# Kernel optimization log

Measured on AMD Instinct MI355X. Metric: run time of the kernel, lower is better.

Reference implementation:

```python
import jax, jax.numpy as jnp
import numpy as np

L, N, E, H, D = 2048, 4, 1024, 16, 128  # seq, batch, embed, heads, proj_dim
HD = E // H                             # head_dim = 64
SIGMA = 1.0
EPS = 1e-6


def setup_inputs() -> dict:
    key = jax.random.key(0)
    ks = jax.random.split(key, 13)
    w = lambda i, shape: jax.random.normal(ks[i], shape, jnp.float32) * 0.02
    return {
        "query": jax.random.normal(ks[0], (L, N, E), jnp.float32),
        "key": jax.random.normal(ks[1], (L, N, E), jnp.float32),
        "value": jax.random.normal(ks[2], (L, N, E), jnp.float32),
        "wq": w(3, (E, E)), "bq": jnp.zeros((E,), jnp.float32),
        "wk": w(4, (E, E)), "bk": jnp.zeros((E,), jnp.float32),
        "wv": w(5, (E, E)), "bv": jnp.zeros((E,), jnp.float32),
        "wo": w(6, (E, E)), "bo": jnp.zeros((E,), jnp.float32),
        "random_matrices": SIGMA * jax.random.normal(ks[7], (H, D, HD), jnp.float32),
    }


def random_project(x, rm):
    # x: (L, N, H, HD), rm: (H, D, HD) -> phi: (N*H, L, 2D)
    scale = 1.0 / np.sqrt(2 * D).astype(np.float32)
    xn = x / jnp.maximum(jnp.linalg.norm(x, axis=-1, keepdims=True), 1e-12)
    xt = jnp.einsum('lnhe,hde->lnhd', xn, rm)
    phi = scale * jnp.concatenate([jnp.exp(xt), jnp.exp(-xt)], axis=-1)  # (L,N,H,2D)
    # faithful to torch .contiguous().view(-1, L, 2D): plain row-major reshape
    return phi.reshape(N * H, L, 2 * D)


def causal_product(phi_q, phi_k, v):
    # phi_q, phi_k: (B, L, 2D); v: (B, L, HD)
    B = phi_q.shape[0]
    def step(carry, inp):
        S, z = carry            # S: (B, 2D, HD) running kv; z: (B, 2D) running k-sum
        qk, kk, vv = inp        # (B, 2D), (B, 2D), (B, HD)
        S = S + kk[:, :, None] * vv[:, None, :]
        z = z + kk
        num = jnp.einsum('bd,bdh->bh', qk, S)
        den = jnp.einsum('bd,bd->b', qk, z)
        return (S, z), num / (den[:, None] + EPS)
    init = (jnp.zeros((B, 2 * D, HD), phi_q.dtype), jnp.zeros((B, 2 * D), phi_q.dtype))
    xs = (jnp.swapaxes(phi_q, 0, 1), jnp.swapaxes(phi_k, 0, 1), jnp.swapaxes(v, 0, 1))
    _, out = jax.lax.scan(step, init, xs)   # out: (L, B, HD)
    return jnp.swapaxes(out, 0, 1)          # (B, L, HD)


def reference(query, key, value, wq, bq, wk, bk, wv, bv, wo, bo, random_matrices):
    q = query @ wq.T + bq
    k = key @ wk.T + bk
    v = value @ wv.T + bv
    q = q.reshape(L, N, H, HD)
    k = k.reshape(L, N, H, HD)
    v = jnp.swapaxes(v.reshape(L, N * H, HD), 0, 1)   # (B=N*H, L, HD)
    phi_q = random_project(q, random_matrices)        # (B, L, 2D)
    phi_k = random_project(k, random_matrices)
    attn = causal_product(phi_q, phi_k, v)            # (B, L, HD)
    attn = jnp.swapaxes(attn, 0, 1).reshape(L, N, E)
    return attn @ wo.T + bo
```

## Files before the change

kernel.cpp:

```cpp
#include <hip/hip_runtime.h>
#include <math.h>


typedef unsigned short u16;
typedef unsigned int u32;
using f32x4v  = __attribute__((ext_vector_type(4))) float;
using f32x16v = __attribute__((ext_vector_type(16))) float;
using s16x8   = __attribute__((ext_vector_type(8))) short;

__device__ __forceinline__ float bf2f(u16 u) { return __uint_as_float(((u32)u) << 16); }
__device__ __forceinline__ u16 f2bf(float x) {
    u32 b = __float_as_uint(x);
    b += 0x7fff + ((b >> 16) & 1);
    return (u16)(b >> 16);
}
__device__ __forceinline__ u32 cvtpk(float lo, float hi) {
    u32 r;
    asm("v_cvt_pk_bf16_f32 %0, %1, %2" : "=v"(r) : "v"(lo), "v"(hi));
    return r;
}
__device__ __forceinline__ float exp2f_hw(float x) {
    float r;
    asm("v_exp_f32 %0, %1" : "=v"(r) : "v"(x));
    return r;
}
__device__ __forceinline__ void gload_lds16(const void* g, void* l) {
    __builtin_amdgcn_global_load_lds(
        (const __attribute__((address_space(1))) void*)g,
        (__attribute__((address_space(3))) void*)l, 16, 0, 0);
}

__global__ __launch_bounds__(256) void cvt_consts(
    const float* __restrict__ w0, const float* __restrict__ w1,
    const float* __restrict__ w2, const float* __restrict__ w3,
    const float* __restrict__ rm, const float* __restrict__ query,
    const float* __restrict__ key, u16* __restrict__ wqkv,
    u16* __restrict__ wob, u16* __restrict__ rmb,
    u16* __restrict__ xq, u16* __restrict__ xk)
{
    const int y = blockIdx.y;
    const float* src;
    u16* d;
    int nblk;
    switch (y) {
        case 0: src = w0; d = wqkv;            nblk = 512;  break;
        case 1: src = w1; d = wqkv + 1048576;  nblk = 512;  break;
        case 2: src = w2; d = wqkv + 2097152;  nblk = 512;  break;
        case 3: src = w3; d = wob;             nblk = 512;  break;
        case 4: src = rm; d = rmb;             nblk = 64;   break;
        case 5: src = query; d = xq;           nblk = 4096; break;
        default: src = key; d = xk;            nblk = 4096; break;
    }
    if ((int)blockIdx.x >= nblk) return;
    const size_t i = ((size_t)blockIdx.x * 256 + threadIdx.x) * 8;
    const float4 a = *(const float4*)(src + i);
    const float4 b = *(const float4*)(src + i + 4);
    u16 o[8] = {f2bf(a.x), f2bf(a.y), f2bf(a.z), f2bf(a.w),
                f2bf(b.x), f2bf(b.y), f2bf(b.z), f2bf(b.w)};
    *(uint4*)(d + i) = *(uint4*)o;
}

__global__ __launch_bounds__(256) void gemm_qkv(
    const u16* __restrict__ XQ, const u16* __restrict__ XK, const float* __restrict__ Xv,
    const u16* __restrict__ WB, const float* __restrict__ bq, const float* __restrict__ bk,
    const float* __restrict__ bv, u16* __restrict__ qp, u16* __restrict__ kp, u16* __restrict__ vpt)
{
    __shared__ __align__(16) u16 As[8192];
    __shared__ __align__(16) u16 Bs[8192];
    const int z = blockIdx.z;
    const u16* Bw = WB + (size_t)z * 1048576;
    const float* bias = (z == 0) ? bq : (z == 1) ? bk : bv;

    const int t = threadIdx.x;
    const int m0 = blockIdx.x * 128, n0 = blockIdx.y * 128;
    const int wid = t >> 6, lane = t & 63;
    const int wr = wid >> 1, wc = wid & 1;
    const int l15 = lane & 15, l4 = lane >> 4;

    f32x4v acc[4][4];
#pragma unroll
    for (int i = 0; i < 4; ++i)
#pragma unroll
        for (int j = 0; j < 4; ++j)
#pragma unroll
            for (int e = 0; e < 4; ++e) acc[i][j][e] = 0.f;

    const int grow = wid * 32 + (lane >> 3);
    const int lcol = ((lane & 7) ^ (lane >> 3)) * 8;
    const u16* gbB = Bw + (size_t)(n0 + grow) * 1024 + lcol;
    const u16* XA  = (z == 0) ? XQ : XK;
    const u16* gaA = XA + (size_t)(m0 + grow) * 1024 + lcol;
    const int srow = t >> 1;
    const int half = t & 1;
    const float* gsrcA = Xv + (size_t)(m0 + srow) * 1024 + half * 32;

    for (int k0 = 0; k0 < 1024; k0 += 64) {
        __syncthreads();
#pragma unroll
        for (int i = 0; i < 4; ++i)
            gload_lds16(gbB + (size_t)i * 8 * 1024 + k0, &Bs[(wid * 32 + i * 8) * 64]);
        if (z < 2) {
#pragma unroll
            for (int i = 0; i < 4; ++i)
                gload_lds16(gaA + (size_t)i * 8 * 1024 + k0, &As[(wid * 32 + i * 8) * 64]);
        } else {
            u16 ta[32];
#pragma unroll
            for (int q = 0; q < 8; ++q) {
                const float4 v = *(const float4*)(gsrcA + k0 + q * 4);
                ta[q*4+0] = f2bf(v.x); ta[q*4+1] = f2bf(v.y);
                ta[q*4+2] = f2bf(v.z); ta[q*4+3] = f2bf(v.w);
            }
#pragma unroll
            for (int q = 0; q < 4; ++q) {
                const int phys = (half * 4 + q) ^ (srow & 7);
                *(uint4*)&As[srow * 64 + phys * 8] = *(const uint4*)&ta[q * 8];
            }
        }
        __syncthreads();
#pragma unroll
        for (int ks = 0; ks < 2; ++ks) {
            s16x8 af[4], bfr[4];
#pragma unroll
            for (int fi = 0; fi < 4; ++fi) {
                const int r = wr * 64 + fi * 16 + l15;
                const int phys = (ks * 4 + l4) ^ (r & 7);
                af[fi] = *(const s16x8*)&As[r * 64 + phys * 8];
            }
#pragma unroll
            for (int fj = 0; fj < 4; ++fj) {
                const int r = wc * 64 + fj * 16 + l15;
                const int phys = (ks * 4 + l4) ^ (r & 7);
                bfr[fj] = *(const s16x8*)&Bs[r * 64 + phys * 8];
            }
#pragma unroll
            for (int fi = 0; fi < 4; ++fi)
#pragma unroll
                for (int fj = 0; fj < 4; ++fj)
                    acc[fi][fj] = __builtin_amdgcn_mfma_f32_16x16x32_bf16(af[fi], bfr[fj], acc[fi][fj], 0, 0, 0);
        }
    }

    u16* Cp = (z == 0) ? qp : (z == 1) ? kp : vpt;
    const int rl = l4 * 4, cl = l15;
    float bvals[4];
#pragma unroll
    for (int fj = 0; fj < 4; ++fj) bvals[fj] = bias[n0 + wc * 64 + fj * 16 + cl];
#pragma unroll
    for (int fi = 0; fi < 4; ++fi)
#pragma unroll
        for (int j = 0; j < 4; ++j) {
            const size_t m = m0 + wr * 64 + fi * 16 + rl + j;
#pragma unroll
            for (int fj = 0; fj < 4; ++fj) {
                const int n = n0 + wc * 64 + fj * 16 + cl;
                const float v = acc[fi][fj][j] + bvals[fj];
                if (z < 2) Cp[m * 1024 + n] = f2bf(v);
                else       Cp[((size_t)((m & 3) * 16 + (n >> 6)) * 64 + (n & 63)) * 2048 + (m >> 2)] = f2bf(v);
            }
        }
}

__global__ __launch_bounds__(256) void gemm_o(
    const u16* __restrict__ A, const u16* __restrict__ Bw,
    const float* __restrict__ bias, float* __restrict__ Cp)
{
    __shared__ __align__(16) u16 As[8192];
    __shared__ __align__(16) u16 Bs[8192];
    const int t = threadIdx.x;
    const int m0 = blockIdx.x * 128, n0 = blockIdx.y * 128;
    const int wid = t >> 6, lane = t & 63;
    const int wr = wid >> 1, wc = wid & 1;
    const int l15 = lane & 15, l4 = lane >> 4;

    f32x4v acc[4][4];
#pragma unroll
    for (int i = 0; i < 4; ++i)
#pragma unroll
        for (int j = 0; j < 4; ++j)
#pragma unroll
            for (int e = 0; e < 4; ++e) acc[i][j][e] = 0.f;

    const int grow = wid * 32 + (lane >> 3);
    const int lcol = ((lane & 7) ^ (lane >> 3)) * 8;
    const u16* gaA = A  + (size_t)(m0 + grow) * 1024 + lcol;
    const u16* gbB = Bw + (size_t)(n0 + grow) * 1024 + lcol;

    for (int k0 = 0; k0 < 1024; k0 += 64) {
        __syncthreads();
#pragma unroll
        for (int i = 0; i < 4; ++i) {
            gload_lds16(gaA + (size_t)i * 8 * 1024 + k0, &As[(wid * 32 + i * 8) * 64]);
            gload_lds16(gbB + (size_t)i * 8 * 1024 + k0, &Bs[(wid * 32 + i * 8) * 64]);
        }
        __syncthreads();
#pragma unroll
        for (int ks = 0; ks < 2; ++ks) {
            s16x8 af[4], bfr[4];
#pragma unroll
            for (int fi = 0; fi < 4; ++fi) {
                const int r = wr * 64 + fi * 16 + l15;
                const int phys = (ks * 4 + l4) ^ (r & 7);
                af[fi] = *(const s16x8*)&As[r * 64 + phys * 8];
            }
#pragma unroll
            for (int fj = 0; fj < 4; ++fj) {
                const int r = wc * 64 + fj * 16 + l15;
                const int phys = (ks * 4 + l4) ^ (r & 7);
                bfr[fj] = *(const s16x8*)&Bs[r * 64 + phys * 8];
            }
#pragma unroll
            for (int fi = 0; fi < 4; ++fi)
#pragma unroll
                for (int fj = 0; fj < 4; ++fj)
                    acc[fi][fj] = __builtin_amdgcn_mfma_f32_16x16x32_bf16(af[fi], bfr[fj], acc[fi][fj], 0, 0, 0);
        }
    }

    const int rl = l4 * 4, cl = l15;
    float bvals[4];
#pragma unroll
    for (int fj = 0; fj < 4; ++fj) bvals[fj] = bias[n0 + wc * 64 + fj * 16 + cl];
#pragma unroll
    for (int fi = 0; fi < 4; ++fi)
#pragma unroll
        for (int j = 0; j < 4; ++j) {
            const size_t m = m0 + wr * 64 + fi * 16 + rl + j;
#pragma unroll
            for (int fj = 0; fj < 4; ++fj) {
                const int n = n0 + wc * 64 + fj * 16 + cl;
                Cp[m * 1024 + n] = acc[fi][fj][j] + bvals[fj];
            }
        }
}

__global__ __launch_bounds__(256) void rand_project_mfma(
    const u16* __restrict__ QP, const u16* __restrict__ KP,
    const u16* __restrict__ RMB, u16* __restrict__ PHIQ, u16* __restrict__ PHIK)
{
    const u16* X  = (blockIdx.z == 0) ? QP : KP;
    u16* PHI      = (blockIdx.z == 0) ? PHIQ : PHIK;
    __shared__ __align__(16) u16 Xs[128 * 72];
    __shared__ __align__(16) u16 RMs[128 * 72];
    __shared__ float rsl_lds[128];
    const int h  = blockIdx.x;
    const int r0 = blockIdx.y * 128;
    const int t  = threadIdx.x;
    const int w  = t >> 6, lane = t & 63;
    const int l15 = lane & 15, l4 = lane >> 4;

    float sq[4];
#pragma unroll
    for (int i = 0; i < 4; ++i) {
        const int lin = t + i * 256;
        const int row = lin >> 3, oct = lin & 7;
        const uint4 xv = *(const uint4*)(X + (size_t)(r0 + row) * 1024 + h * 64 + oct * 8);
        *(uint4*)&Xs[row * 72 + oct * 8] = xv;
        const u16* pv = (const u16*)&xv;
        float s = 0.f;
#pragma unroll
        for (int e = 0; e < 8; ++e) { const float f = bf2f(pv[e]); s += f * f; }
        sq[i] = s;
        const uint4 rv = *(const uint4*)(RMB + (size_t)h * 8192 + lin * 8);
        *(uint4*)&RMs[row * 72 + oct * 8] = rv;
    }
#pragma unroll
    for (int i = 0; i < 4; ++i) {
        sq[i] += __shfl_xor(sq[i], 1);
        sq[i] += __shfl_xor(sq[i], 2);
        sq[i] += __shfl_xor(sq[i], 4);
        if ((t & 7) == 0)
            rsl_lds[(t >> 3) + i * 32] = 1.4426950408889634f / fmaxf(sqrtf(sq[i]), 1e-12f);
    }
    __syncthreads();

    const int wr = (w >> 1) * 64, wc = (w & 1) * 64;
    f32x4v acc[4][4];
#pragma unroll
    for (int i = 0; i < 4; ++i)
#pragma unroll
        for (int j = 0; j < 4; ++j)
#pragma unroll
            for (int e = 0; e < 4; ++e) acc[i][j][e] = 0.f;
#pragma unroll
    for (int ks = 0; ks < 2; ++ks) {
        s16x8 af[4], bfr[4];
#pragma unroll
        for (int fi = 0; fi < 4; ++fi)
            af[fi] = *(const s16x8*)&Xs[(wr + fi * 16 + l15) * 72 + ks * 32 + l4 * 8];
#pragma unroll
        for (int fj = 0; fj < 4; ++fj)
            bfr[fj] = *(const s16x8*)&RMs[(wc + fj * 16 + l15) * 72 + ks * 32 + l4 * 8];
#pragma unroll
        for (int fi = 0; fi < 4; ++fi)
#pragma unroll
            for (int fj = 0; fj < 4; ++fj)
                acc[fi][fj] = __builtin_amdgcn_mfma_f32_16x16x32_bf16(af[fi], bfr[fj], acc[fi][fj], 0, 0, 0);
    }

#pragma unroll
    for (int fi = 0; fi < 4; ++fi)
#pragma unroll
        for (int reg = 0; reg < 4; ++reg) {
            const int row = wr + fi * 16 + l4 * 4 + reg;
            const float rsl = rsl_lds[row];
            const size_t base = ((size_t)(r0 + row) * 16 + h) * 256;
#pragma unroll
            for (int fj = 0; fj < 4; ++fj) {
                const int d = wc + fj * 16 + l15;
                const float arg = acc[fi][fj][reg] * rsl;
                PHI[base + d]       = f2bf(exp2f_hw(arg - 4.f));
                PHI[base + 128 + d] = f2bf(exp2f_hw(-arg - 4.f));
            }
        }
}

__global__ __launch_bounds__(256) void chunk_state_mfma(
    const u16* __restrict__ PHIK, const u16* __restrict__ VPT, u16* __restrict__ STC)
{
    __shared__ __align__(16) u16 Ks[64 * 136];
    __shared__ float zlds[16][132];
    const int b = blockIdx.x;
    const int c = blockIdx.y >> 1;
    const int dh = blockIdx.y & 1;
    const int t = threadIdx.x;
    const int wid = t >> 6, lane = t & 63;
    const int l15 = lane & 15, l4 = lane >> 4;
    const int wr = wid >> 1, wc = wid & 1;

    const size_t R0 = (size_t)b * 2048 + (size_t)c * 256;
    const int rgrp = t >> 4, d08 = (t & 15) * 8;

    float zpart[8];
#pragma unroll
    for (int i = 0; i < 8; ++i) zpart[i] = 0.f;

    f32x4v acc[2][4];
#pragma unroll
    for (int i = 0; i < 2; ++i)
#pragma unroll
        for (int j = 0; j < 4; ++j)
#pragma unroll
            for (int e = 0; e < 4; ++e) acc[i][j][e] = 0.f;

    for (int stage = 0; stage < 4; ++stage) {
        __syncthreads();
#pragma unroll
        for (int j = 0; j < 4; ++j) {
            const int r = rgrp + 16 * j;
            const uint4 v = *(const uint4*)(PHIK + (R0 + stage * 64 + r) * 256 + dh * 128 + d08);
            const int x = ((r >> 3) & 3) << 1;
            *(uint4*)&Ks[r * 136 + (((d08 >> 3) ^ x) << 3)] = v;
            const u16* pv = (const u16*)&v;
#pragma unroll
            for (int i = 0; i < 8; ++i) zpart[i] += bf2f(pv[i]);
        }
        __syncthreads();
#pragma unroll
        for (int ks = 0; ks < 2; ++ks) {
            const int xk = ((ks * 4 + l4) & 3) << 1;
            const int r0 = ks * 32 + l4 * 8;
            s16x8 af[2], bk[4];
#pragma unroll
            for (int fi = 0; fi < 2; ++fi) {
                const int h = wr * 32 + fi * 16 + l15;
                af[fi] = *(const s16x8*)(VPT + ((size_t)b * 64 + h) * 2048 + c * 256 + stage * 64 + ks * 32 + l4 * 8);
            }
#pragma unroll
            for (int fj = 0; fj < 4; ++fj) {
                const int d = wc * 64 + fj * 16 + l15;
                const int colk = (((d >> 3) ^ xk) << 3) + (d & 7);
#pragma unroll
                for (int e = 0; e < 8; ++e)
                    bk[fj][e] = (short)Ks[(r0 + e) * 136 + colk];
            }
#pragma unroll
            for (int fi = 0; fi < 2; ++fi)
#pragma unroll
                for (int fj = 0; fj < 4; ++fj)
                    acc[fi][fj] = __builtin_amdgcn_mfma_f32_16x16x32_bf16(af[fi], bk[fj], acc[fi][fj], 0, 0, 0);
        }
    }
    __syncthreads();
    *(float4*)&zlds[rgrp][d08]     = *(float4*)&zpart[0];
    *(float4*)&zlds[rgrp][d08 + 4] = *(float4*)&zpart[4];
    __syncthreads();
    u16* st = STC + (size_t)(b * 8 + c) * 16640;
    if (t < 128) {
        float z = 0.f;
#pragma unroll
        for (int g = 0; g < 16; ++g) z += zlds[g][t];
        st[16384 + dh * 128 + t] = f2bf(z);
    }
#pragma unroll
    for (int fi = 0; fi < 2; ++fi)
#pragma unroll
        for (int reg = 0; reg < 4; ++reg) {
            const int h = wr * 32 + fi * 16 + l4 * 4 + reg;
#pragma unroll
            for (int fj = 0; fj < 4; ++fj) {
                const int d = dh * 128 + wc * 64 + fj * 16 + l15;
                st[(size_t)h * 256 + d] = f2bf(acc[fi][fj][reg]);
            }
        }
}

__global__ void prefix_scan(const u16* __restrict__ STC, u16* __restrict__ STBF)
{
    const int b = blockIdx.x;
    const int e = blockIdx.y * 256 + threadIdx.x;
    if (e >= 16640) return;
    float run = 0.f;
#pragma unroll
    for (int c = 0; c < 8; ++c) {
        const size_t idx = (size_t)(b * 8 + c) * 16640 + e;
        const float v = bf2f(STC[idx]);
        STBF[idx] = f2bf(run);
        run += v;
    }
}

__global__ __launch_bounds__(128) void causal_fused(
    const u16* __restrict__ PHIQ, const u16* __restrict__ PHIK,
    const u16* __restrict__ VPT, const u16* __restrict__ STBF,
    u16* __restrict__ ATT)
{
    const u32 bid = blockIdx.x;
    const int pair = (int)((bid >> 3) & 3);
    const int G  = (int)((bid >> 5) * 8 + (bid & 7));
    const int b  = G & 63;
    const int c  = G >> 6;
    const int w  = threadIdx.x >> 6;
    const int rf = w ? (7 - pair) : pair;
    const int ri = rf >> 1, fi = rf & 1;
    const int lane = threadIdx.x & 63;
    const int l31 = lane & 31, s = lane >> 5;
    const size_t chunk0 = (size_t)b * 2048 + (size_t)c * 256;
    const u16* stb = STBF + (size_t)(b * 8 + c) * 16640;

    const int qc = ri * 64 + fi * 32 + l31;
    s16x8 qf[16];
    const u16* qp = PHIQ + (chunk0 + qc) * 256 + s * 8;
#pragma unroll
    for (int ds = 0; ds < 16; ++ds)
        qf[ds] = *(const s16x8*)(qp + ds * 16);

    f32x16v o[2], o2;
#pragma unroll
    for (int e = 0; e < 16; ++e) { o[0][e] = 0.f; o[1][e] = 0.f; o2[e] = 0.f; }
    float den = 0.f;

#pragma unroll
    for (int ds = 0; ds < 16; ++ds) {
        const s16x8 zf = *(const s16x8*)(stb + 16384 + ds * 16 + s * 8);
        o2 = __builtin_amdgcn_mfma_f32_32x32x16_bf16(qf[ds], zf, o2, 0, 0, 0);
#pragma unroll
        for (int fh = 0; fh < 2; ++fh) {
            const s16x8 sx = *(const s16x8*)(stb + (fh * 32 + l31) * 256 + ds * 16 + s * 8);
            o[fh] = __builtin_amdgcn_mfma_f32_32x32x16_bf16(qf[ds], sx, o[fh], 0, 0, 0);
        }
    }

    const int kbmax = ri * 2 + fi;
    for (int kb = 0; kb <= kbmax; ++kb) {
        s16x8 vf[2][2];
#pragma unroll
        for (int kh = 0; kh < 2; ++kh)
#pragma unroll
            for (int fh = 0; fh < 2; ++fh)
                vf[kh][fh] = *(const s16x8*)(VPT + ((size_t)b * 64 + fh * 32 + l31) * 2048
                                             + c * 256 + kb * 32 + kh * 16 + s * 8);
        f32x16v p0, p1;
#pragma unroll
        for (int e = 0; e < 16; ++e) { p0[e] = 0.f; p1[e] = 0.f; }
        const u16* kptr = PHIK + (chunk0 + kb * 32 + l31) * 256 + s * 8;
#pragma unroll
        for (int ds = 0; ds < 8; ++ds) {
            const s16x8 kf0 = *(const s16x8*)(kptr + (2 * ds) * 16);
            const s16x8 kf1 = *(const s16x8*)(kptr + (2 * ds + 1) * 16);
            p0 = __builtin_amdgcn_mfma_f32_32x32x16_bf16(kf0, qf[2 * ds],     p0, 0, 0, 0);
            p1 = __builtin_amdgcn_mfma_f32_32x32x16_bf16(kf1, qf[2 * ds + 1], p1, 0, 0, 0);
        }
        f32x16v p;
#pragma unroll
        for (int e = 0; e < 16; ++e) p[e] = p0[e] + p1[e];

        const bool diag = (kb == kbmax);
        float rsum = 0.f;
#pragma unroll
        for (int reg = 0; reg < 16; ++reg) {
            if (diag) {
                const int kc = kb * 32 + (reg & 3) + 8 * (reg >> 2) + 4 * s;
                if (kc > qc) p[reg] = 0.f;
            }
            rsum += p[reg];
        }
        den += rsum;
#pragma unroll
        for (int kh = 0; kh < 2; ++kh) {
            const u32 pA_lo = cvtpk(p[8*kh + 0], p[8*kh + 1]);
            const u32 pA_hi = cvtpk(p[8*kh + 2], p[8*kh + 3]);
            const u32 pB_lo = cvtpk(p[8*kh + 4], p[8*kh + 5]);
            const u32 pB_hi = cvtpk(p[8*kh + 6], p[8*kh + 7]);
            const u32 X_lo = s ? pB_lo : pA_lo;
            const u32 X_hi = s ? pB_hi : pA_hi;
            const u32 Y_lo = s ? pA_lo : pB_lo;
            const u32 Y_hi = s ? pA_hi : pB_hi;
            const u32 sY_lo = __shfl_xor((int)Y_lo, 32);
            const u32 sY_hi = __shfl_xor((int)Y_hi, 32);
            u32 wq[4];
            wq[0] = s ? sY_lo : X_lo;
            wq[1] = s ? sY_hi : X_hi;
            wq[2] = s ? X_lo : sY_lo;
            wq[3] = s ? X_hi : sY_hi;
            s16x8 pa;
#pragma unroll
            for (int i = 0; i < 4; ++i) {
                pa[2*i]   = (short)(wq[i] & 0xffff);
                pa[2*i+1] = (short)(wq[i] >> 16);
            }
            o[0] = __builtin_amdgcn_mfma_f32_32x32x16_bf16(pa, vf[kh][0], o[0], 0, 0, 0);
            o[1] = __builtin_amdgcn_mfma_f32_32x32x16_bf16(pa, vf[kh][1], o[1], 0, 0, 0);
        }
    }

    const float denT = den + __shfl_xor(den, 32);
#pragma unroll
    for (int reg = 0; reg < 16; ++reg) {
        const int q32 = (reg & 3) + 8 * (reg >> 2) + 4 * s;
        const float dv = o2[reg] + __shfl(denT, q32);
        const float inv = 1.f / (dv + 1e-6f);
        const int qrow = c * 256 + ri * 64 + fi * 32 + q32;
        const size_t abase = (size_t)qrow * 4096 + b * 64;
        ATT[abase + l31]      = f2bf(o[0][reg] * inv);
        ATT[abase + 32 + l31] = f2bf(o[1][reg] * inv);
    }
}

extern "C" void kernel_launch(void* const* d_in, const int* in_sizes, int n_in,
                              void* d_out, int out_size, void* d_ws, size_t ws_size,
                              hipStream_t stream)
{
    const float* query = (const float*)d_in[0];
    const float* key   = (const float*)d_in[1];
    const float* value = (const float*)d_in[2];
    const float* wq    = (const float*)d_in[3];
    const float* bq    = (const float*)d_in[4];
    const float* wk    = (const float*)d_in[5];
    const float* bk    = (const float*)d_in[6];
    const float* wv    = (const float*)d_in[7];
    const float* bv    = (const float*)d_in[8];
    const float* wo    = (const float*)d_in[9];
    const float* bo    = (const float*)d_in[10];
    const float* rm    = (const float*)d_in[11];
    float* out = (float*)d_out;

    char* base = (char*)d_ws;
    u16* phiq = (u16*)(base);
    u16* phik = (u16*)(base +  67108864);
    u16* vpt  = (u16*)(base + 134217728);
    u16* qp   = (u16*)(base + 150994944);
    u16* kp   = (u16*)(base + 167772160);
    u16* stc  = (u16*)(base + 184549376);
    u16* stbf = (u16*)(base + 201588736);
    u16* xq   = (u16*)(base + 184549376);
    u16* xk   = (u16*)(base + 201326592);
    u16* wob  = (u16*)(base + 218628096);
    u16* rmb  = (u16*)(base + 220725248);
    u16* wqkv = phiq;
    u16* attn = qp;

    const dim3 blk(256);
    cvt_consts<<<dim3(4096, 7), blk, 0, stream>>>(wq, wk, wv, wo, rm, query, key,
                                                  wqkv, wob, rmb, xq, xk);
    gemm_qkv<<<dim3(64, 8, 3), blk, 0, stream>>>(xq, xk, value, wqkv, bq, bk, bv, qp, kp, vpt);
    rand_project_mfma<<<dim3(16, 64, 2), blk, 0, stream>>>(qp, kp, rmb, phiq, phik);
    chunk_state_mfma<<<dim3(64, 16), blk, 0, stream>>>(phik, vpt, stc);
    prefix_scan<<<dim3(64, 65), blk, 0, stream>>>(stc, stbf);
    causal_fused<<<dim3(2048), dim3(128), 0, stream>>>(phiq, phik, vpt, stbf, attn);
    gemm_o<<<dim3(64, 8), blk, 0, stream>>>(attn, wob, bo, out);
}
```

Before: 279.2 us.

## Fuse random-feature projection into the QKV GEMM epilogue

Removes the separate rand_project kernel. The Q and K projection blocks now normalise their 64-wide head slices in registers, stage them in LDS, and run the random-matrix MFMA plus exp in the epilogue, writing phi directly. This drops the bf16 qp/kp round trip through global memory and one kernel launch. In exchange the GEMM epilogue gets heavier and uses more LDS, random matrices are read straight from global memory per wave, and the workspace layout moves wqkv to a new offset.

```diff
diff --git a/kernel.cpp b/kernel.cpp
--- a/kernel.cpp
+++ b/kernel.cpp
@@ -63,10 +63,12 @@
 __global__ __launch_bounds__(256) void gemm_qkv(
     const u16* __restrict__ XQ, const u16* __restrict__ XK, const float* __restrict__ Xv,
     const u16* __restrict__ WB, const float* __restrict__ bq, const float* __restrict__ bk,
-    const float* __restrict__ bv, u16* __restrict__ qp, u16* __restrict__ kp, u16* __restrict__ vpt)
-{
-    __shared__ __align__(16) u16 As[8192];
-    __shared__ __align__(16) u16 Bs[8192];
+    const float* __restrict__ bv, const u16* __restrict__ RMB,
+    u16* __restrict__ PHIQ, u16* __restrict__ PHIK, u16* __restrict__ vpt)
+{
+    __shared__ __align__(16) u16 sm[18432];
+    u16* As = sm;
+    u16* Bs = sm + 8192;
     const int z = blockIdx.z;
     const u16* Bw = WB + (size_t)z * 1048576;
     const float* bias = (z == 0) ? bq : (z == 1) ? bk : bv;
@@ -141,24 +143,91 @@
         }
     }
 
-    u16* Cp = (z == 0) ? qp : (z == 1) ? kp : vpt;
-    const int rl = l4 * 4, cl = l15;
     float bvals[4];
 #pragma unroll
-    for (int fj = 0; fj < 4; ++fj) bvals[fj] = bias[n0 + wc * 64 + fj * 16 + cl];
+    for (int fj = 0; fj < 4; ++fj) bvals[fj] = bias[n0 + wc * 64 + fj * 16 + l15];
+
+    if (z == 2) {
+#pragma unroll
+        for (int fi = 0; fi < 4; ++fi)
+#pragma unroll
+            for (int j = 0; j < 4; ++j) {
+                const size_t m = m0 + wr * 64 + fi * 16 + l4 * 4 + j;
+#pragma unroll
+                for (int fj = 0; fj < 4; ++fj) {
+                    const int n = n0 + wc * 64 + fj * 16 + l15;
+                    vpt[((size_t)((m & 3) * 16 + (n >> 6)) * 64 + (n & 63)) * 2048 + (m >> 2)]
+                        = f2bf(acc[fi][fj][j] + bvals[fj]);
+                }
+            }
+        return;
+    }
+
+    __syncthreads();
+    const int h = blockIdx.y * 2 + wc;
+    u16* Xw = sm + wid * 4608;
+    u16* PHI = (z == 0) ? PHIQ : PHIK;
+
+    float rsl[4][4];
 #pragma unroll
     for (int fi = 0; fi < 4; ++fi)
 #pragma unroll
         for (int j = 0; j < 4; ++j) {
-            const size_t m = m0 + wr * 64 + fi * 16 + rl + j;
+            float s = 0.f;
 #pragma unroll
             for (int fj = 0; fj < 4; ++fj) {
-                const int n = n0 + wc * 64 + fj * 16 + cl;
-                const float v = acc[fi][fj][j] + bvals[fj];
-                if (z < 2) Cp[m * 1024 + n] = f2bf(v);
-                else       Cp[((size_t)((m & 3) * 16 + (n >> 6)) * 64 + (n & 63)) * 2048 + (m >> 2)] = f2bf(v);
-            }
-        }
+                const u16 xb = f2bf(acc[fi][fj][j] + bvals[fj]);
+                Xw[(fi * 16 + l4 * 4 + j) * 72 + fj * 16 + l15] = xb;
+                const float xf = bf2f(xb);
+                s += xf * xf;
+            }
+            s += __shfl_xor(s, 1);
+            s += __shfl_xor(s, 2);
+            s += __shfl_xor(s, 4);
+            s += __shfl_xor(s, 8);
+            rsl[fi][j] = 1.4426950408889634f / fmaxf(sqrtf(s), 1e-12f);
+        }
+
+#pragma unroll
+    for (int dh = 0; dh < 2; ++dh) {
+        f32x4v p2[4][4];
+#pragma unroll
+        for (int i = 0; i < 4; ++i)
+#pragma unroll
+            for (int j = 0; j < 4; ++j)
+#pragma unroll
+                for (int e = 0; e < 4; ++e) p2[i][j][e] = 0.f;
+#pragma unroll
+        for (int ks = 0; ks < 2; ++ks) {
+            s16x8 xa[4];
+#pragma unroll
+            for (int fi = 0; fi < 4; ++fi)
+                xa[fi] = *(const s16x8*)&Xw[(fi * 16 + l15) * 72 + ks * 32 + l4 * 8];
+#pragma unroll
+            for (int fjd = 0; fjd < 4; ++fjd) {
+                const int d = dh * 64 + fjd * 16 + l15;
+                const s16x8 rb = *(const s16x8*)(RMB + (size_t)h * 8192 + d * 64 + ks * 32 + l4 * 8);
+#pragma unroll
+                for (int fi = 0; fi < 4; ++fi)
+                    p2[fi][fjd] = __builtin_amdgcn_mfma_f32_16x16x32_bf16(xa[fi], rb, p2[fi][fjd], 0, 0, 0);
+            }
+        }
+#pragma unroll
+        for (int fi = 0; fi < 4; ++fi)
+#pragma unroll
+            for (int reg = 0; reg < 4; ++reg) {
+                const size_t m = m0 + wr * 64 + fi * 16 + l4 * 4 + reg;
+                const size_t pb = (m * 16 + h) * 256;
+                const float r = rsl[fi][reg];
+#pragma unroll
+                for (int fjd = 0; fjd < 4; ++fjd) {
+                    const int d = dh * 64 + fjd * 16 + l15;
+                    const float arg = p2[fi][fjd][reg] * r;
+                    PHI[pb + d]       = f2bf(exp2f_hw(arg - 4.f));
+                    PHI[pb + 128 + d] = f2bf(exp2f_hw(-arg - 4.f));
+                }
+            }
+    }
 }
 
 __global__ __launch_bounds__(256) void gemm_o(
@@ -230,87 +299,6 @@
             for (int fj = 0; fj < 4; ++fj) {
                 const int n = n0 + wc * 64 + fj * 16 + cl;
                 Cp[m * 1024 + n] = acc[fi][fj][j] + bvals[fj];
-            }
-        }
-}
-
-__global__ __launch_bounds__(256) void rand_project_mfma(
-    const u16* __restrict__ QP, const u16* __restrict__ KP,
-    const u16* __restrict__ RMB, u16* __restrict__ PHIQ, u16* __restrict__ PHIK)
-{
-    const u16* X  = (blockIdx.z == 0) ? QP : KP;
-    u16* PHI      = (blockIdx.z == 0) ? PHIQ : PHIK;
-    __shared__ __align__(16) u16 Xs[128 * 72];
-    __shared__ __align__(16) u16 RMs[128 * 72];
-    __shared__ float rsl_lds[128];
-    const int h  = blockIdx.x;
-    const int r0 = blockIdx.y * 128;
-    const int t  = threadIdx.x;
-    const int w  = t >> 6, lane = t & 63;
-    const int l15 = lane & 15, l4 = lane >> 4;
-
-    float sq[4];
-#pragma unroll
-    for (int i = 0; i < 4; ++i) {
-        const int lin = t + i * 256;
-        const int row = lin >> 3, oct = lin & 7;
-        const uint4 xv = *(const uint4*)(X + (size_t)(r0 + row) * 1024 + h * 64 + oct * 8);
-        *(uint4*)&Xs[row * 72 + oct * 8] = xv;
-        const u16* pv = (const u16*)&xv;
-        float s = 0.f;
-#pragma unroll
-        for (int e = 0; e < 8; ++e) { const float f = bf2f(pv[e]); s += f * f; }
-        sq[i] = s;
-        const uint4 rv = *(const uint4*)(RMB + (size_t)h * 8192 + lin * 8);
-        *(uint4*)&RMs[row * 72 + oct * 8] = rv;
-    }
-#pragma unroll
-    for (int i = 0; i < 4; ++i) {
-        sq[i] += __shfl_xor(sq[i], 1);
-        sq[i] += __shfl_xor(sq[i], 2);
-        sq[i] += __shfl_xor(sq[i], 4);
-        if ((t & 7) == 0)
-            rsl_lds[(t >> 3) + i * 32] = 1.4426950408889634f / fmaxf(sqrtf(sq[i]), 1e-12f);
-    }
-    __syncthreads();
-
-    const int wr = (w >> 1) * 64, wc = (w & 1) * 64;
-    f32x4v acc[4][4];
-#pragma unroll
-    for (int i = 0; i < 4; ++i)
-#pragma unroll
-        for (int j = 0; j < 4; ++j)
-#pragma unroll
-            for (int e = 0; e < 4; ++e) acc[i][j][e] = 0.f;
-#pragma unroll
-    for (int ks = 0; ks < 2; ++ks) {
-        s16x8 af[4], bfr[4];
-#pragma unroll
-        for (int fi = 0; fi < 4; ++fi)
-            af[fi] = *(const s16x8*)&Xs[(wr + fi * 16 + l15) * 72 + ks * 32 + l4 * 8];
-#pragma unroll
-        for (int fj = 0; fj < 4; ++fj)
-            bfr[fj] = *(const s16x8*)&RMs[(wc + fj * 16 + l15) * 72 + ks * 32 + l4 * 8];
-#pragma unroll
-        for (int fi = 0; fi < 4; ++fi)
-#pragma unroll
-            for (int fj = 0; fj < 4; ++fj)
-                acc[fi][fj] = __builtin_amdgcn_mfma_f32_16x16x32_bf16(af[fi], bfr[fj], acc[fi][fj], 0, 0, 0);
-    }
-
-#pragma unroll
-    for (int fi = 0; fi < 4; ++fi)
-#pragma unroll
-        for (int reg = 0; reg < 4; ++reg) {
-            const int row = wr + fi * 16 + l4 * 4 + reg;
-            const float rsl = rsl_lds[row];
-            const size_t base = ((size_t)(r0 + row) * 16 + h) * 256;
-#pragma unroll
-            for (int fj = 0; fj < 4; ++fj) {
-                const int d = wc + fj * 16 + l15;
-                const float arg = acc[fi][fj][reg] * rsl;
-                PHI[base + d]       = f2bf(exp2f_hw(arg - 4.f));
-                PHI[base + 128 + d] = f2bf(exp2f_hw(-arg - 4.f));
             }
         }
 }
@@ -559,22 +547,20 @@
     u16* phiq = (u16*)(base);
     u16* phik = (u16*)(base +  67108864);
     u16* vpt  = (u16*)(base + 134217728);
-    u16* qp   = (u16*)(base + 150994944);
-    u16* kp   = (u16*)(base + 167772160);
+    u16* attn = (u16*)(base + 150994944);
     u16* stc  = (u16*)(base + 184549376);
     u16* stbf = (u16*)(base + 201588736);
     u16* xq   = (u16*)(base + 184549376);
     u16* xk   = (u16*)(base + 201326592);
     u16* wob  = (u16*)(base + 218628096);
     u16* rmb  = (u16*)(base + 220725248);
-    u16* wqkv = phiq;
-    u16* attn = qp;
+    u16* wqkv = (u16*)(base + 220987392);
 
     const dim3 blk(256);
     cvt_consts<<<dim3(4096, 7), blk, 0, stream>>>(wq, wk, wv, wo, rm, query, key,
                                                   wqkv, wob, rmb, xq, xk);
-    gemm_qkv<<<dim3(64, 8, 3), blk, 0, stream>>>(xq, xk, value, wqkv, bq, bk, bv, qp, kp, vpt);
-    rand_project_mfma<<<dim3(16, 64, 2), blk, 0, stream>>>(qp, kp, rmb, phiq, phik);
+    gemm_qkv<<<dim3(64, 8, 3), blk, 0, stream>>>(xq, xk, value, wqkv, bq, bk, bv,
+                                                 rmb, phiq, phik, vpt);
     chunk_state_mfma<<<dim3(64, 16), blk, 0, stream>>>(phik, vpt, stc);
     prefix_scan<<<dim3(64, 65), blk, 0, stream>>>(stc, stbf);
     causal_fused<<<dim3(2048), dim3(128), 0, stream>>>(phiq, phik, vpt, stbf, attn);
```

Result: slower. 342.4 us (+22.6%).
